# Kernel optimization log

Measured on AMD Instinct MI355X. Metric: run time of the kernel, lower is better.

The kernel has to match this reference:

```python
import jax, jax.numpy as jnp
import numpy as np

K = 8   # heads
d = 8   # per-head dim
D = K * d  # 64


def setup_inputs() -> dict:
    key = jax.random.key(0)
    ks = jax.random.split(key, 12)
    B, T, N = 8, 12, 512
    s2 = 1.0 / np.sqrt(2 * D)
    s1 = 1.0 / np.sqrt(D)
    return {
        "X": jax.random.normal(ks[0], (B, T, N, D), jnp.float32),
        "STE": jax.random.normal(ks[1], (B, T, N, D), jnp.float32),
        "W7": jax.random.uniform(ks[2], (2 * D, D), jnp.float32, -s2, s2),
        "b7": jnp.zeros((D,), jnp.float32),
        "W8": jax.random.uniform(ks[3], (2 * D, D), jnp.float32, -s2, s2),
        "b8": jnp.zeros((D,), jnp.float32),
        "W9": jax.random.uniform(ks[4], (2 * D, D), jnp.float32, -s2, s2),
        "b9": jnp.zeros((D,), jnp.float32),
        "W10": jax.random.uniform(ks[5], (D, D), jnp.float32, -s1, s1),
        "b10": jnp.zeros((D,), jnp.float32),
        "W11": jax.random.uniform(ks[6], (D, D), jnp.float32, -s1, s1),
        "b11": jnp.zeros((D,), jnp.float32),
    }


def _heads(x):
    # torch.cat(torch.split(x, d, -1), 0): [B,T,N,D] -> [K,B,T,N,d] (head-major batch)
    B, T, N, _ = x.shape
    return jnp.moveaxis(x.reshape(B, T, N, K, d), 3, 0)


def reference(X, STE, W7, b7, W8, b8, W9, b9, W10, b10, W11, b11):
    H = jnp.concatenate([X, STE], axis=-1)                 # [B,T,N,2D]
    q = _heads(jax.nn.relu(H @ W7 + b7))                   # [K,B,T,N,d]
    k = _heads(jax.nn.relu(H @ W8 + b8))
    v = _heads(jax.nn.relu(H @ W9 + b9))
    scores = jnp.einsum('kbtnd,kbtmd->kbtnm', q, k) / jnp.sqrt(jnp.float32(d))
    attn = jax.nn.softmax(scores, axis=-1)                 # [K,B,T,N,N]
    out = jnp.einsum('kbtnm,kbtmd->kbtnd', attn, v)        # [K,B,T,N,d]
    # torch.cat(torch.split(out, B, 0), -1): [K,B,T,N,d] -> [B,T,N,K*d]
    Kk, B, T, N, _ = out.shape
    out = jnp.moveaxis(out, 0, 3).reshape(B, T, N, D)
    return jax.nn.relu(out @ W10 + b10) @ W11 + b11
```

## Files before the change

kernel.cpp:

```cpp
#include <hip/hip_runtime.h>
#include <hip/hip_bf16.h>
#include <math.h>

#define BT    96
#define NSEQ  512
#define DMODEL 64
#define RTOT  (BT * NSEQ)

#define QOFF  0
#define KOFF  ((size_t)RTOT * DMODEL)
#define VOFF  ((size_t)2 * RTOT * DMODEL)
#define OOFF  ((size_t)3 * RTOT * DMODEL)
#define WOFF  ((size_t)4 * RTOT * DMODEL)

static __device__ inline float fast_exp2(float x) {
#if __has_builtin(__builtin_amdgcn_exp2f)
    return __builtin_amdgcn_exp2f(x);
#else
    float r; asm("v_exp_f32 %0, %1" : "=v"(r) : "v"(x)); return r;
#endif
}
static __device__ inline float fast_rcp(float x) {
#if __has_builtin(__builtin_amdgcn_rcpf)
    return __builtin_amdgcn_rcpf(x);
#else
    return 1.f / x;
#endif
}

typedef __attribute__((ext_vector_type(8)))  short short8;
typedef __attribute__((ext_vector_type(16))) float float16v;

static __device__ inline short8 as_s8(uint4 u) {
    union { uint4 u; short8 s; } x; x.u = u; return x.s;
}

static __device__ inline uint32_t bf162_bits(__hip_bfloat162 h) {
    union { __hip_bfloat162 h; uint32_t u; } x; x.h = h; return x.u;
}

static __device__ inline void split_pack8(const float* v, uint4* hi, uint4* lo) {
    uint32_t h[4], l[4];
    #pragma unroll
    for (int t = 0; t < 4; ++t) {
        float x0 = v[2 * t], x1 = v[2 * t + 1];
        uint32_t hw = bf162_bits(__float22bfloat162_rn(make_float2(x0, x1)));
        float h0 = __uint_as_float(hw << 16);
        float h1 = __uint_as_float(hw & 0xffff0000u);
        h[t] = hw;
        float l0 = x0 - h0;
        float l1 = x1 - h1;
        l[t] = bf162_bits(__float22bfloat162_rn(make_float2(l0, l1)));
    }
    *hi = make_uint4(h[0], h[1], h[2], h[3]);
    *lo = make_uint4(l[0], l[1], l[2], l[3]);
}

__global__ __launch_bounds__(256) void wprep_kernel(
    const float* __restrict__ W7, const float* __restrict__ W8,
    const float* __restrict__ W9, const float* __restrict__ W10,
    const float* __restrict__ W11,
    uint4* __restrict__ WfH, uint4* __restrict__ WfL)
{
    const int e = blockIdx.x * 256 + threadIdx.x;
    const float* W;
    int k0, col;
    if (e < 3072) {
        int n  = e & 31;
        int t  = (e >> 5) & 1;
        int hh = (e >> 6) & 1;
        int c  = (e >> 7) & 7;
        int w  = e >> 10;
        W = (w == 0) ? W7 : (w == 1) ? W8 : W9;
        k0 = c * 16 + hh * 8;
        col = t * 32 + n;
    } else {
        int pe = e - 3072;
        int n  = pe & 31;
        int t  = (pe >> 5) & 1;
        int hh = (pe >> 6) & 1;
        int c  = (pe >> 7) & 3;
        int m  = pe >> 9;
        W = (m == 0) ? W10 : W11;
        k0 = c * 16 + hh * 8;
        col = t * 32 + n;
    }
    float v[8];
    #pragma unroll
    for (int j = 0; j < 8; ++j) v[j] = W[(size_t)(k0 + j) * 64 + col];
    uint4 hi, lo;
    split_pack8(v, &hi, &lo);
    WfH[e] = hi;
    WfL[e] = lo;
}

__global__ __launch_bounds__(192) void qkv_kernel(
    const float* __restrict__ X, const float* __restrict__ STE,
    const uint4* __restrict__ WfH, const uint4* __restrict__ WfL,
    const float* __restrict__ b7, const float* __restrict__ b8,
    const float* __restrict__ b9,
    float* __restrict__ qkv)
{
    __shared__ uint4 aH[512];
    __shared__ uint4 aL[512];

    const int tid  = threadIdx.x;
    const int l31  = tid & 31;
    const int hh   = (tid >> 5) & 1;
    const int w    = tid >> 6;
    const size_t blockrow = (size_t)blockIdx.x * 32;

    for (int e = tid; e < 512; e += 192) {
        const int el  = e & 31;
        const int ehh = (e >> 5) & 1;
        const int ec  = e >> 6;
        const float* src = (ec < 4) ? X : STE;
        const float* ap = src + (blockrow + el) * 64 + (ec & 3) * 16 + ehh * 8;
        float av[8];
        {
            float4 a0 = *(const float4*)(ap);
            float4 a1 = *(const float4*)(ap + 4);
            av[0] = a0.x; av[1] = a0.y; av[2] = a0.z; av[3] = a0.w;
            av[4] = a1.x; av[5] = a1.y; av[6] = a1.z; av[7] = a1.w;
        }
        uint4 hi, lo;
        split_pack8(av, &hi, &lo);
        aH[e] = hi;
        aL[e] = lo;
    }
    __syncthreads();

    float16v accM[2], accC[2];
    #pragma unroll
    for (int t = 0; t < 2; ++t)
        #pragma unroll
        for (int i = 0; i < 16; ++i) { accM[t][i] = 0.f; accC[t][i] = 0.f; }

    #pragma unroll
    for (int c = 0; c < 8; ++c) {
        const uint4 ahi = aH[c * 64 + hh * 32 + l31];
        const uint4 alo = aL[c * 64 + hh * 32 + l31];

        #pragma unroll
        for (int t = 0; t < 2; ++t) {
            const int ei = w * 1024 + c * 128 + hh * 64 + t * 32 + l31;
            const uint4 bh = WfH[ei];
            const uint4 bl = WfL[ei];
            accM[t] = __builtin_amdgcn_mfma_f32_32x32x16_bf16(
                as_s8(ahi), as_s8(bh), accM[t], 0, 0, 0);
            accC[t] = __builtin_amdgcn_mfma_f32_32x32x16_bf16(
                as_s8(alo), as_s8(bh), accC[t], 0, 0, 0);
            accC[t] = __builtin_amdgcn_mfma_f32_32x32x16_bf16(
                as_s8(ahi), as_s8(bl), accC[t], 0, 0, 0);
        }
    }

    const float* bv = (w == 0) ? b7 : (w == 1) ? b8 : b9;
    float* obase = qkv + (size_t)w * ((size_t)RTOT * DMODEL);
    #pragma unroll
    for (int t = 0; t < 2; ++t) {
        const int col = t * 32 + l31;
        const float bias = bv[col];
        #pragma unroll
        for (int r = 0; r < 16; ++r) {
            const int rowC = (r & 3) + 8 * (r >> 2) + 4 * hh;
            obase[(blockrow + rowC) * 64 + col] =
                fmaxf(accM[t][r] + accC[t][r] + bias, 0.f);
        }
    }
}

__global__ __launch_bounds__(512, 4) void attn_kernel(
    const float* __restrict__ qkv, float* __restrict__ obuf)
{
    __shared__ uint4 ak1[16 * 32];
    __shared__ uint4 ak2p[16 * 33];
    __shared__ uint4 vfh[640];
    __shared__ uint4 vfl[640];

    const int tid  = threadIdx.x;
    const int lane = tid & 63;
    const int l31  = lane & 31;
    const int hh   = lane >> 5;
    const int wv   = tid >> 6;
    const int head = blockIdx.x & 7;
    const int bt   = blockIdx.x >> 3;

    const size_t rowbase = (size_t)bt * NSEQ * 64 + (size_t)head * 8;
    const float* Qp = qkv + QOFF + rowbase;
    const float* Kp = qkv + KOFF + rowbase;
    const float* Vp = qkv + VOFF + rowbase;

    const uint4 z4 = make_uint4(0, 0, 0, 0);

    {
        const int k = tid;
        const float* kr = Kp + (size_t)k * 64;
        float kv[8];
        float4 a = *(const float4*)(kr);
        float4 b = *(const float4*)(kr + 4);
        kv[0] = a.x; kv[1] = a.y; kv[2] = a.z; kv[3] = a.w;
        kv[4] = b.x; kv[5] = b.y; kv[6] = b.z; kv[7] = b.w;
        uint4 hi, lo;
        split_pack8(kv, &hi, &lo);
        ak1[k] = hi;
        ak2p[(k >> 5) * 33 + (k & 31)] = lo;
    }
    if (tid < 16) ak2p[tid * 33 + 32] = z4;

    for (int e = tid; e < 640; e += 512) {
        if (e < 576) {
            int s  = e / 18;
            int r  = e % 18;
            int hv = r / 9;
            int n  = r % 9;
            float vv[8];
            #pragma unroll
            for (int j = 0; j < 8; ++j) {
                int key = 16 * s + ((j < 4) ? (4 * hv + j) : (8 + 4 * hv + (j - 4)));
                vv[j] = (n < 8) ? Vp[(size_t)key * 64 + n] : 1.0f;
            }
            uint4 hi, lo;
            split_pack8(vv, &hi, &lo);
            vfh[e] = hi;
            vfl[e] = lo;
        } else {
            vfh[e] = z4;
            vfl[e] = z4;
        }
    }

    __syncthreads();

    const float C = 0.51012091684045906f;
    const int idx2 = hh ? 32 : l31;

    float16v Z16;
    #pragma unroll
    for (int i = 0; i < 16; ++i) Z16[i] = 0.f;

    for (int qt = wv; qt < 16; qt += 8) {
        const float* qp = Qp + (size_t)(qt * 32 + l31) * 64;
        float qv[8];
        {
            float4 a = *(const float4*)(qp);
            float4 b = *(const float4*)(qp + 4);
            qv[0] = a.x * C; qv[1] = a.y * C; qv[2] = a.z * C; qv[3] = a.w * C;
            qv[4] = b.x * C; qv[5] = b.y * C; qv[6] = b.z * C; qv[7] = b.w * C;
        }
        uint4 qhi, qlo;
        split_pack8(qv, &qhi, &qlo);
        const uint4 bq1 = hh ? qlo : qhi;
        const uint4 bq2 = qhi;

        float16v Oa = Z16, Ob = Z16;

        for (int c = 0; c < 16; ++c) {
            const uint4 a1 = ak1[c * 32 + l31];
            const uint4 a2 = ak2p[c * 33 + idx2];
            const int vi0 = (4 * c + hh) * 9;
            const int vi1 = (4 * c + 2 + hh) * 9;
            const uint4 bh0 = vfh[vi0 + l31];
            const uint4 bl0 = vfl[vi0 + l31];
            const uint4 bh1 = vfh[vi1 + l31];
            const uint4 bl1 = vfl[vi1 + l31];

            float16v S;
            S = __builtin_amdgcn_mfma_f32_32x32x16_bf16(as_s8(a1), as_s8(bq1), Z16, 0, 0, 0);
            S = __builtin_amdgcn_mfma_f32_32x32x16_bf16(as_s8(a2), as_s8(bq2), S, 0, 0, 0);

            float pv[16];
            #pragma unroll
            for (int i = 0; i < 16; ++i) pv[i] = fast_exp2(S[i]);

            uint4 ph0, pl0, ph1, pl1;
            split_pack8(&pv[0], &ph0, &pl0);
            split_pack8(&pv[8], &ph1, &pl1);

            Oa = __builtin_amdgcn_mfma_f32_32x32x16_bf16(as_s8(ph0), as_s8(bh0), Oa, 0, 0, 0);
            Ob = __builtin_amdgcn_mfma_f32_32x32x16_bf16(as_s8(ph1), as_s8(bh1), Ob, 0, 0, 0);
            Oa = __builtin_amdgcn_mfma_f32_32x32x16_bf16(as_s8(pl0), as_s8(bh0), Oa, 0, 0, 0);
            Ob = __builtin_amdgcn_mfma_f32_32x32x16_bf16(as_s8(pl1), as_s8(bh1), Ob, 0, 0, 0);
            Oa = __builtin_amdgcn_mfma_f32_32x32x16_bf16(as_s8(ph0), as_s8(bl0), Oa, 0, 0, 0);
            Ob = __builtin_amdgcn_mfma_f32_32x32x16_bf16(as_s8(ph1), as_s8(bl1), Ob, 0, 0, 0);
        }

        #pragma unroll
        for (int r = 0; r < 16; ++r) {
            float ov = Oa[r] + Ob[r];
            float den = __uint_as_float(
                __builtin_amdgcn_ds_swizzle(__float_as_uint(ov), 0x100));
            float o = ov * fast_rcp(den);
            if (l31 < 8) {
                int row = (r & 3) + 8 * (r >> 2) + 4 * hh;
                obuf[rowbase + (size_t)(qt * 32 + row) * 64 + l31] = o;
            }
        }
    }
}

__global__ __launch_bounds__(64) void proj_kernel(
    const float* __restrict__ obuf,
    const uint4* __restrict__ WfH, const uint4* __restrict__ WfL,
    const float* __restrict__ b10, const float* __restrict__ b11,
    float* __restrict__ out)
{
    __shared__ float Ts[32][68];

    const int lane = threadIdx.x;
    const int l31  = lane & 31;
    const int hh   = lane >> 5;
    const size_t row = (size_t)blockIdx.x * 32 + l31;
    const size_t blockrow = (size_t)blockIdx.x * 32;

    float16v accM[2], accC[2];
    #pragma unroll
    for (int t = 0; t < 2; ++t)
        #pragma unroll
        for (int i = 0; i < 16; ++i) { accM[t][i] = 0.f; accC[t][i] = 0.f; }

    #pragma unroll
    for (int c = 0; c < 4; ++c) {
        const float* ap = obuf + row * 64 + c * 16 + hh * 8;
        float av[8];
        {
            float4 a0 = *(const float4*)(ap);
            float4 a1 = *(const float4*)(ap + 4);
            av[0] = a0.x; av[1] = a0.y; av[2] = a0.z; av[3] = a0.w;
            av[4] = a1.x; av[5] = a1.y; av[6] = a1.z; av[7] = a1.w;
        }
        uint4 ahi, alo;
        split_pack8(av, &ahi, &alo);

        #pragma unroll
        for (int t = 0; t < 2; ++t) {
            const int ei = 3072 + c * 128 + hh * 64 + t * 32 + l31;
            const uint4 bh = WfH[ei];
            const uint4 bl = WfL[ei];
            accM[t] = __builtin_amdgcn_mfma_f32_32x32x16_bf16(
                as_s8(ahi), as_s8(bh), accM[t], 0, 0, 0);
            accC[t] = __builtin_amdgcn_mfma_f32_32x32x16_bf16(
                as_s8(alo), as_s8(bh), accC[t], 0, 0, 0);
            accC[t] = __builtin_amdgcn_mfma_f32_32x32x16_bf16(
                as_s8(ahi), as_s8(bl), accC[t], 0, 0, 0);
        }
    }

    #pragma unroll
    for (int t = 0; t < 2; ++t) {
        const int col = t * 32 + l31;
        const float bias = b10[col];
        #pragma unroll
        for (int r = 0; r < 16; ++r) {
            const int rowC = (r & 3) + 8 * (r >> 2) + 4 * hh;
            Ts[rowC][col] = fmaxf(accM[t][r] + accC[t][r] + bias, 0.f);
        }
    }
    __syncthreads();

    #pragma unroll
    for (int t = 0; t < 2; ++t)
        #pragma unroll
        for (int i = 0; i < 16; ++i) { accM[t][i] = 0.f; accC[t][i] = 0.f; }

    #pragma unroll
    for (int c = 0; c < 4; ++c) {
        const float* ap = &Ts[l31][c * 16 + hh * 8];
        float av[8];
        {
            float4 a0 = *(const float4*)(ap);
            float4 a1 = *(const float4*)(ap + 4);
            av[0] = a0.x; av[1] = a0.y; av[2] = a0.z; av[3] = a0.w;
            av[4] = a1.x; av[5] = a1.y; av[6] = a1.z; av[7] = a1.w;
        }
        uint4 ahi, alo;
        split_pack8(av, &ahi, &alo);

        #pragma unroll
        for (int t = 0; t < 2; ++t) {
            const int ei = 3584 + c * 128 + hh * 64 + t * 32 + l31;
            const uint4 bh = WfH[ei];
            const uint4 bl = WfL[ei];
            accM[t] = __builtin_amdgcn_mfma_f32_32x32x16_bf16(
                as_s8(ahi), as_s8(bh), accM[t], 0, 0, 0);
            accC[t] = __builtin_amdgcn_mfma_f32_32x32x16_bf16(
                as_s8(alo), as_s8(bh), accC[t], 0, 0, 0);
            accC[t] = __builtin_amdgcn_mfma_f32_32x32x16_bf16(
                as_s8(ahi), as_s8(bl), accC[t], 0, 0, 0);
        }
    }

    #pragma unroll
    for (int t = 0; t < 2; ++t) {
        const int col = t * 32 + l31;
        const float bias = b11[col];
        #pragma unroll
        for (int r = 0; r < 16; ++r) {
            const int rowC = (r & 3) + 8 * (r >> 2) + 4 * hh;
            out[(blockrow + rowC) * 64 + col] = accM[t][r] + accC[t][r] + bias;
        }
    }
}

extern "C" void kernel_launch(void* const* d_in, const int* in_sizes, int n_in,
                              void* d_out, int out_size, void* d_ws, size_t ws_size,
                              hipStream_t stream)
{
    const float* X   = (const float*)d_in[0];
    const float* STE = (const float*)d_in[1];
    const float* W7  = (const float*)d_in[2];
    const float* b7  = (const float*)d_in[3];
    const float* W8  = (const float*)d_in[4];
    const float* b8  = (const float*)d_in[5];
    const float* W9  = (const float*)d_in[6];
    const float* b9  = (const float*)d_in[7];
    const float* W10 = (const float*)d_in[8];
    const float* b10 = (const float*)d_in[9];
    const float* W11 = (const float*)d_in[10];
    const float* b11 = (const float*)d_in[11];

    float* ws  = (float*)d_ws;
    float* out = (float*)d_out;

    uint4* WfH = (uint4*)(ws + WOFF);
    uint4* WfL = WfH + 4096;

    wprep_kernel<<<dim3(16), 256, 0, stream>>>(W7, W8, W9, W10, W11, WfH, WfL);
    qkv_kernel<<<dim3(RTOT / 32), 192, 0, stream>>>(X, STE, WfH, WfL, b7, b8, b9, ws);
    attn_kernel<<<dim3(BT * 8), 512, 0, stream>>>(ws, ws + OOFF);
    proj_kernel<<<dim3(RTOT / 32), 64, 0, stream>>>(ws + OOFF, WfH, WfL, b10, b11, out);
}
```

Baseline: 183.2 us.

## Software-pipeline QK^T MFMA in attention and split projection column tiles across waves

In the attention loop, the score MFMAs for the next key chunk are issued before the exp2 and PV MFMAs of the current chunk, so matrix-core latency overlaps the exp work. The loop is unrolled by two. The qkv and proj kernels now give each wave one 32-column tile instead of two, doubling waves per block to add parallelism and cut per-wave accumulator registers. The attention pipelining raises register pressure and computes one extra wrapped score tile per query tile.

```diff
diff --git a/kernel.cpp b/kernel.cpp
--- a/kernel.cpp
+++ b/kernel.cpp
@@ -94,7 +94,7 @@
     WfL[e] = lo;
 }
 
-__global__ __launch_bounds__(192) void qkv_kernel(
+__global__ __launch_bounds__(384) void qkv_kernel(
     const float* __restrict__ X, const float* __restrict__ STE,
     const uint4* __restrict__ WfH, const uint4* __restrict__ WfL,
     const float* __restrict__ b7, const float* __restrict__ b8,
@@ -107,10 +107,12 @@
     const int tid  = threadIdx.x;
     const int l31  = tid & 31;
     const int hh   = (tid >> 5) & 1;
-    const int w    = tid >> 6;
+    const int wave = tid >> 6;
+    const int w    = wave >> 1;
+    const int tt   = wave & 1;
     const size_t blockrow = (size_t)blockIdx.x * 32;
 
-    for (int e = tid; e < 512; e += 192) {
+    for (int e = tid; e < 512; e += 384) {
         const int el  = e & 31;
         const int ehh = (e >> 5) & 1;
         const int ec  = e >> 6;
@@ -130,43 +132,34 @@
     }
     __syncthreads();
 
-    float16v accM[2], accC[2];
-    #pragma unroll
-    for (int t = 0; t < 2; ++t)
-        #pragma unroll
-        for (int i = 0; i < 16; ++i) { accM[t][i] = 0.f; accC[t][i] = 0.f; }
+    float16v accM, accC;
+    #pragma unroll
+    for (int i = 0; i < 16; ++i) { accM[i] = 0.f; accC[i] = 0.f; }
 
     #pragma unroll
     for (int c = 0; c < 8; ++c) {
         const uint4 ahi = aH[c * 64 + hh * 32 + l31];
         const uint4 alo = aL[c * 64 + hh * 32 + l31];
-
-        #pragma unroll
-        for (int t = 0; t < 2; ++t) {
-            const int ei = w * 1024 + c * 128 + hh * 64 + t * 32 + l31;
-            const uint4 bh = WfH[ei];
-            const uint4 bl = WfL[ei];
-            accM[t] = __builtin_amdgcn_mfma_f32_32x32x16_bf16(
-                as_s8(ahi), as_s8(bh), accM[t], 0, 0, 0);
-            accC[t] = __builtin_amdgcn_mfma_f32_32x32x16_bf16(
-                as_s8(alo), as_s8(bh), accC[t], 0, 0, 0);
-            accC[t] = __builtin_amdgcn_mfma_f32_32x32x16_bf16(
-                as_s8(ahi), as_s8(bl), accC[t], 0, 0, 0);
-        }
+        const int ei = w * 1024 + c * 128 + hh * 64 + tt * 32 + l31;
+        const uint4 bh = WfH[ei];
+        const uint4 bl = WfL[ei];
+        accM = __builtin_amdgcn_mfma_f32_32x32x16_bf16(
+            as_s8(ahi), as_s8(bh), accM, 0, 0, 0);
+        accC = __builtin_amdgcn_mfma_f32_32x32x16_bf16(
+            as_s8(alo), as_s8(bh), accC, 0, 0, 0);
+        accC = __builtin_amdgcn_mfma_f32_32x32x16_bf16(
+            as_s8(ahi), as_s8(bl), accC, 0, 0, 0);
     }
 
     const float* bv = (w == 0) ? b7 : (w == 1) ? b8 : b9;
     float* obase = qkv + (size_t)w * ((size_t)RTOT * DMODEL);
-    #pragma unroll
-    for (int t = 0; t < 2; ++t) {
-        const int col = t * 32 + l31;
-        const float bias = bv[col];
-        #pragma unroll
-        for (int r = 0; r < 16; ++r) {
-            const int rowC = (r & 3) + 8 * (r >> 2) + 4 * hh;
-            obase[(blockrow + rowC) * 64 + col] =
-                fmaxf(accM[t][r] + accC[t][r] + bias, 0.f);
-        }
+    const int col = tt * 32 + l31;
+    const float bias = bv[col];
+    #pragma unroll
+    for (int r = 0; r < 16; ++r) {
+        const int rowC = (r & 3) + 8 * (r >> 2) + 4 * hh;
+        obase[(blockrow + rowC) * 64 + col] =
+            fmaxf(accM[r] + accC[r] + bias, 0.f);
     }
 }
 
@@ -255,9 +248,17 @@
 
         float16v Oa = Z16, Ob = Z16;
 
+        float16v S0;
+        {
+            const uint4 a1 = ak1[l31];
+            const uint4 a2 = ak2p[idx2];
+            S0 = __builtin_amdgcn_mfma_f32_32x32x16_bf16(as_s8(a1), as_s8(bq1), Z16, 0, 0, 0);
+            S0 = __builtin_amdgcn_mfma_f32_32x32x16_bf16(as_s8(a2), as_s8(bq2), S0, 0, 0, 0);
+        }
+
+        #pragma unroll 2
         for (int c = 0; c < 16; ++c) {
-            const uint4 a1 = ak1[c * 32 + l31];
-            const uint4 a2 = ak2p[c * 33 + idx2];
+            const int cn = (c + 1) & 15;
             const int vi0 = (4 * c + hh) * 9;
             const int vi1 = (4 * c + 2 + hh) * 9;
             const uint4 bh0 = vfh[vi0 + l31];
@@ -265,14 +266,18 @@
             const uint4 bh1 = vfh[vi1 + l31];
             const uint4 bl1 = vfl[vi1 + l31];
 
-            float16v S;
-            S = __builtin_amdgcn_mfma_f32_32x32x16_bf16(as_s8(a1), as_s8(bq1), Z16, 0, 0, 0);
-            S = __builtin_amdgcn_mfma_f32_32x32x16_bf16(as_s8(a2), as_s8(bq2), S, 0, 0, 0);
+            const uint4 a1n = ak1[cn * 32 + l31];
+            const uint4 a2n = ak2p[cn * 33 + idx2];
+            float16v S1;
+            S1 = __builtin_amdgcn_mfma_f32_32x32x16_bf16(as_s8(a1n), as_s8(bq1), Z16, 0, 0, 0);
+            S1 = __builtin_amdgcn_mfma_f32_32x32x16_bf16(as_s8(a2n), as_s8(bq2), S1, 0, 0, 0);
+
+            #pragma unroll
+            for (int i = 0; i < 16; ++i) S0[i] = fast_exp2(S0[i]);
 
             float pv[16];
             #pragma unroll
-            for (int i = 0; i < 16; ++i) pv[i] = fast_exp2(S[i]);
-
+            for (int i = 0; i < 16; ++i) pv[i] = S0[i];
             uint4 ph0, pl0, ph1, pl1;
             split_pack8(&pv[0], &ph0, &pl0);
             split_pack8(&pv[8], &ph1, &pl1);
@@ -283,6 +288,8 @@
             Ob = __builtin_amdgcn_mfma_f32_32x32x16_bf16(as_s8(pl1), as_s8(bh1), Ob, 0, 0, 0);
             Oa = __builtin_amdgcn_mfma_f32_32x32x16_bf16(as_s8(ph0), as_s8(bl0), Oa, 0, 0, 0);
             Ob = __builtin_amdgcn_mfma_f32_32x32x16_bf16(as_s8(ph1), as_s8(bl1), Ob, 0, 0, 0);
+
+            S0 = S1;
         }
 
         #pragma unroll
@@ -299,25 +306,25 @@
     }
 }
 
-__global__ __launch_bounds__(64) void proj_kernel(
+__global__ __launch_bounds__(128) void proj_kernel(
     const float* __restrict__ obuf,
     const uint4* __restrict__ WfH, const uint4* __restrict__ WfL,
     const float* __restrict__ b10, const float* __restrict__ b11,
     float* __restrict__ out)
 {
-    __shared__ float Ts[32][68];
-
-    const int lane = threadIdx.x;
+    __shared__ float Ts[32][80];
+
+    const int tid  = threadIdx.x;
+    const int lane = tid & 63;
     const int l31  = lane & 31;
     const int hh   = lane >> 5;
+    const int tw   = tid >> 6;
     const size_t row = (size_t)blockIdx.x * 32 + l31;
     const size_t blockrow = (size_t)blockIdx.x * 32;
 
-    float16v accM[2], accC[2];
-    #pragma unroll
-    for (int t = 0; t < 2; ++t)
-        #pragma unroll
-        for (int i = 0; i < 16; ++i) { accM[t][i] = 0.f; accC[t][i] = 0.f; }
+    float16v accM, accC;
+    #pragma unroll
+    for (int i = 0; i < 16; ++i) { accM[i] = 0.f; accC[i] = 0.f; }
 
     #pragma unroll
     for (int c = 0; c < 4; ++c) {
@@ -332,36 +339,30 @@
         uint4 ahi, alo;
         split_pack8(av, &ahi, &alo);
 
-        #pragma unroll
-        for (int t = 0; t < 2; ++t) {
-            const int ei = 3072 + c * 128 + hh * 64 + t * 32 + l31;
-            const uint4 bh = WfH[ei];
-            const uint4 bl = WfL[ei];
-            accM[t] = __builtin_amdgcn_mfma_f32_32x32x16_bf16(
-                as_s8(ahi), as_s8(bh), accM[t], 0, 0, 0);
-            accC[t] = __builtin_amdgcn_mfma_f32_32x32x16_bf16(
-                as_s8(alo), as_s8(bh), accC[t], 0, 0, 0);
-            accC[t] = __builtin_amdgcn_mfma_f32_32x32x16_bf16(
-                as_s8(ahi), as_s8(bl), accC[t], 0, 0, 0);
-        }
-    }
-
-    #pragma unroll
-    for (int t = 0; t < 2; ++t) {
-        const int col = t * 32 + l31;
+        const int ei = 3072 + c * 128 + hh * 64 + tw * 32 + l31;
+        const uint4 bh = WfH[ei];
+        const uint4 bl = WfL[ei];
+        accM = __builtin_amdgcn_mfma_f32_32x32x16_bf16(
+            as_s8(ahi), as_s8(bh), accM, 0, 0, 0);
+        accC = __builtin_amdgcn_mfma_f32_32x32x16_bf16(
+            as_s8(alo), as_s8(bh), accC, 0, 0, 0);
+        accC = __builtin_amdgcn_mfma_f32_32x32x16_bf16(
+            as_s8(ahi), as_s8(bl), accC, 0, 0, 0);
+    }
+
+    {
+        const int col = tw * 32 + l31;
         const float bias = b10[col];
         #pragma unroll
         for (int r = 0; r < 16; ++r) {
             const int rowC = (r & 3) + 8 * (r >> 2) + 4 * hh;
-            Ts[rowC][col] = fmaxf(accM[t][r] + accC[t][r] + bias, 0.f);
+            Ts[rowC][col] = fmaxf(accM[r] + accC[r] + bias, 0.f);
         }
     }
     __syncthreads();
 
     #pragma unroll
-    for (int t = 0; t < 2; ++t)
-        #pragma unroll
-        for (int i = 0; i < 16; ++i) { accM[t][i] = 0.f; accC[t][i] = 0.f; }
+    for (int i = 0; i < 16; ++i) { accM[i] = 0.f; accC[i] = 0.f; }
 
     #pragma unroll
     for (int c = 0; c < 4; ++c) {
@@ -376,28 +377,24 @@
         uint4 ahi, alo;
         split_pack8(av, &ahi, &alo);
 
-        #pragma unroll
-        for (int t = 0; t < 2; ++t) {
-            const int ei = 3584 + c * 128 + hh * 64 + t * 32 + l31;
-            const uint4 bh = WfH[ei];
-            const uint4 bl = WfL[ei];
-            accM[t] = __builtin_amdgcn_mfma_f32_32x32x16_bf16(
-                as_s8(ahi), as_s8(bh), accM[t], 0, 0, 0);
-            accC[t] = __builtin_amdgcn_mfma_f32_32x32x16_bf16(
-                as_s8(alo), as_s8(bh), accC[t], 0, 0, 0);
-            accC[t] = __builtin_amdgcn_mfma_f32_32x32x16_bf16(
-                as_s8(ahi), as_s8(bl), accC[t], 0, 0, 0);
-        }
-    }
-
-    #pragma unroll
-    for (int t = 0; t < 2; ++t) {
-        const int col = t * 32 + l31;
+        const int ei = 3584 + c * 128 + hh * 64 + tw * 32 + l31;
+        const uint4 bh = WfH[ei];
+        const uint4 bl = WfL[ei];
+        accM = __builtin_amdgcn_mfma_f32_32x32x16_bf16(
+            as_s8(ahi), as_s8(bh), accM, 0, 0, 0);
+        accC = __builtin_amdgcn_mfma_f32_32x32x16_bf16(
+            as_s8(alo), as_s8(bh), accC, 0, 0, 0);
+        accC = __builtin_amdgcn_mfma_f32_32x32x16_bf16(
+            as_s8(ahi), as_s8(bl), accC, 0, 0, 0);
+    }
+
+    {
+        const int col = tw * 32 + l31;
         const float bias = b11[col];
         #pragma unroll
         for (int r = 0; r < 16; ++r) {
             const int rowC = (r & 3) + 8 * (r >> 2) + 4 * hh;
-            out[(blockrow + rowC) * 64 + col] = accM[t][r] + accC[t][r] + bias;
+            out[(blockrow + rowC) * 64 + col] = accM[r] + accC[r] + bias;
         }
     }
 }
@@ -426,7 +423,7 @@
     uint4* WfL = WfH + 4096;
 
     wprep_kernel<<<dim3(16), 256, 0, stream>>>(W7, W8, W9, W10, W11, WfH, WfL);
-    qkv_kernel<<<dim3(RTOT / 32), 192, 0, stream>>>(X, STE, WfH, WfL, b7, b8, b9, ws);
+    qkv_kernel<<<dim3(RTOT / 32), 384, 0, stream>>>(X, STE, WfH, WfL, b7, b8, b9, ws);
     attn_kernel<<<dim3(BT * 8), 512, 0, stream>>>(ws, ws + OOFF);
-    proj_kernel<<<dim3(RTOT / 32), 64, 0, stream>>>(ws + OOFF, WfH, WfL, b10, b11, out);
-}
+    proj_kernel<<<dim3(RTOT / 32), 128, 0, stream>>>(ws + OOFF, WfH, WfL, b10, b11, out);
+}
```

Result: no change. 180.0 us (-1.8%).
